# Kernel tuning notes

Hardware: AMD Instinct MI355X
Metric: run time of the kernel (lower is better)

Reference implementation:

```python
import jax, jax.numpy as jnp
import numpy as np

N, E, G = 20000, 320000, 256      # nodes, edges, graphs per batch
IN, D, P = 128, 256, 16           # input_dim, out_dim, n_prot
EPS, R, TEMP = 1e-7, 0.5, 0.2


def setup_inputs() -> dict:
    key = jax.random.key(0)
    ks = jax.random.split(key, 9)
    x = jax.random.normal(ks[0], (N, IN), jnp.float32)
    edge_index = jax.random.randint(ks[1], (2, E), 0, N)
    batch = jnp.sort(jax.random.randint(ks[2], (N,), 0, G))
    def w(k, sh):
        fan_in = sh[0]
        return jax.random.normal(k, sh, jnp.float32) * (1.0 / fan_in) ** 0.5
    return {
        "x": x, "edge_index": edge_index, "batch": batch,
        "W1": w(ks[3], (IN, D)), "b1": jnp.zeros((D,), jnp.float32),
        "W2": w(ks[4], (D, D)), "b2": jnp.zeros((D,), jnp.float32),
        "Wm1": w(ks[5], (2 * D, D)), "bm1": jnp.zeros((D,), jnp.float32),
        "Wm2": w(ks[6], (D, 1)), "bm2": jnp.zeros((1,), jnp.float32),
        "prototypes": jax.random.normal(ks[7], (P, D), jnp.float32),
    }


def _cosine(a, b):
    # prototype_distances: cosine similarity with zero-norm -> eps fixup (eval path, no softmax)
    na = jnp.linalg.norm(a, axis=1)
    na = jnp.where(na == 0, na + EPS, na)
    nb = jnp.linalg.norm(b, axis=1)
    nb = jnp.where(nb == 0, nb + EPS, nb)
    return jnp.einsum('ik,jk->ij', a, b) / (na[:, None] * nb[None, :])


def _encoder(x, src, dst, batch, W1, b1, W2, b2, atten=None):
    # 2-layer GIN: h' = relu((h + sum_{j->i} atten_ji * h_j) W + b); graph emb = sum pool
    def conv(h, W, b):
        msg = h[src]                                   # [E, d]
        if atten is not None:
            msg = msg * atten                          # [E, 1] broadcast
        agg = h + jax.ops.segment_sum(msg, dst, num_segments=N)
        return jax.nn.relu(agg @ W + b)
    h = conv(x, W1, b1)
    h = conv(h, W2, b2)
    g = jax.ops.segment_sum(h, batch, num_segments=G)  # [G, D]
    return g, h


def reference(x, edge_index, batch, W1, b1, W2, b2, Wm1, bm1, Wm2, bm2, prototypes):
    src, dst = edge_index[0], edge_index[1]
    graph_embs, node_embs = _encoder(x, src, dst, batch, W1, b1, W2, b2)

    # eval path: assign each graph to nearest prototype by cosine similarity
    sim0 = _cosine(graph_embs, prototypes)             # [G, P]
    assign_prot = jnp.argmax(sim0, axis=1)             # [G]

    # sample_subgraph (eval: plain sigmoid, no gumbel noise)
    node_proto = prototypes[assign_prot[batch]]        # [N, D]
    h = jnp.concatenate([node_embs, node_proto], axis=-1)
    node_prob = jax.nn.relu(h @ Wm1 + bm1) @ Wm2 + bm2  # [N, 1]
    node_bern = jax.nn.sigmoid(node_prob)              # [N, 1]
    edge_bern = node_bern[src] * node_bern[dst]        # [E, 1]

    x2 = x * node_bern
    subgraph_embs, _ = _encoder(x2, src, dst, batch, W1, b1, W2, b2, atten=edge_bern)

    similarity = _cosine(subgraph_embs, prototypes)    # [G, P]

    # NCE loss
    a2 = jnp.argmax(similarity, axis=1)
    onehot = jax.nn.one_hot(a2, P, dtype=similarity.dtype)
    se = jnp.exp(similarity / TEMP)
    pos = (se * onehot).sum(axis=1)
    neg = (se * (1.0 - onehot)).sum(axis=1)
    NCE_loss = -jnp.log(pos / neg).mean()

    # KL regularizers
    nb = node_bern
    KL_node = (nb * jnp.log(nb / R + EPS)
               + (1 - nb) * jnp.log((1 - nb) / (1 - R + EPS) + EPS)).mean()
    eb = edge_bern
    KL_edge = (eb * jnp.log(eb / (R * R) + EPS)
               + (1 - eb) * jnp.log((1 - eb) / (1 - R * R + EPS) + EPS)).mean()
    KL_loss = KL_node + KL_edge

    data_sim = _cosine(subgraph_embs, subgraph_embs)   # [G, G]
    return (KL_loss, NCE_loss, similarity, node_bern, edge_bern,
            data_sim, subgraph_embs, node_embs)
```

## Files before the change

kernel.cpp:

```cpp
#include <hip/hip_runtime.h>
#include <cmath>
#include <cstdint>

#define DINL __device__ __forceinline__

namespace {

constexpr int Nn = 20000, Ee = 320000, Gg = 256, Dd = 256, Pp = 16;
constexpr int Npad = 20096;
constexpr float EPSf = 1e-7f, Rf = 0.5f, TEMPf = 0.2f;

typedef unsigned short u16;
typedef __attribute__((ext_vector_type(8))) short short8;
typedef __attribute__((ext_vector_type(4))) float floatx4;
typedef __attribute__((ext_vector_type(2))) unsigned int u2v;
typedef __attribute__((ext_vector_type(4))) unsigned int u4v;

DINL float waveSum(float x) {
#pragma unroll
  for (int off = 32; off > 0; off >>= 1) x += __shfl_xor(x, off, 64);
  return x;
}

DINL u16 f2bf(float f) {
  unsigned u = __float_as_uint(f);
  unsigned r = u + 0x7fffu + ((u >> 16) & 1u);
  return (u16)(r >> 16);
}
DINL float bf2f(u16 h) { return __uint_as_float(((unsigned)h) << 16); }

__global__ void k_setup(const int* __restrict__ dst, int* __restrict__ deg,
                        const float* __restrict__ W1, const float* __restrict__ W2,
                        const float* __restrict__ Wm1, u16* __restrict__ W1th,
                        u16* __restrict__ W1tl, u16* __restrict__ W2th,
                        u16* __restrict__ W2tl, u16* __restrict__ Wm1th,
                        u16* __restrict__ Wm1tl, const float* __restrict__ proto,
                        const float* __restrict__ bm1, float* __restrict__ pcb,
                        float* __restrict__ pnorm, const float* __restrict__ x,
                        u16* __restrict__ xbf, const int* __restrict__ batch,
                        int* __restrict__ goff) {
  const int eB = (Ee + 255) / 256;
  int blk = blockIdx.x;
  int tid = threadIdx.x;
  if (blk < eB) {
    int e = blk * 256 + tid;
    if (e < Ee) atomicAdd(&deg[dst[e]], 1);
  } else if (blk < eB + 640) {
    int idx = (blk - eB) * 256 + tid;
    const float* W;
    u16 *th, *tl;
    int K;
    if (idx < 128 * 256) {
      W = W1; th = W1th; tl = W1tl; K = 128;
    } else if (idx < 128 * 256 + 256 * 256) {
      idx -= 128 * 256;
      W = W2; th = W2th; tl = W2tl; K = 256;
    } else {
      idx -= 128 * 256 + 256 * 256;
      W = Wm1; th = Wm1th; tl = Wm1tl; K = 256;
    }
    int k = idx >> 8, n = idx & 255;
    float v = W[idx];
    u16 h = f2bf(v);
    th[(size_t)n * K + k] = h;
    tl[(size_t)n * K + k] = f2bf(v - bf2f(h));
  } else if (blk < eB + 656) {
    int p = blk - eB - 640;
    float s = bm1[tid];
    for (int k = 0; k < Dd; k++)
      s += proto[p * Dd + k] * Wm1[(size_t)(Dd + k) * Dd + tid];
    pcb[p * Dd + tid] = s;
    if (tid < 64) {
      float4 v = ((const float4*)(proto + (size_t)p * Dd))[tid];
      float nsq = waveSum(v.x * v.x + v.y * v.y + v.z * v.z + v.w * v.w);
      if (tid == 0) {
        float n = sqrtf(nsq);
        pnorm[p] = (n == 0.f) ? EPSf : n;
      }
    }
  } else if (blk < eB + 656 + 2500) {
    int i = (blk - eB - 656) * 256 + tid;
    if (i < Nn * 128 / 4) {
      float4 v = ((const float4*)x)[i];
      u2v o;
      o.x = (unsigned)f2bf(v.x) | ((unsigned)f2bf(v.y) << 16);
      o.y = (unsigned)f2bf(v.z) | ((unsigned)f2bf(v.w) << 16);
      __builtin_nontemporal_store(o, (u2v*)&xbf[(size_t)i * 4]);
    }
  } else {
    for (int i = tid; i < Nn; i += 256) {
      int bi = batch[i];
      int bp = (i == 0) ? -1 : batch[i - 1];
      for (int g = bp + 1; g <= bi; ++g) goff[g] = i;
      if (i == Nn - 1)
        for (int g = bi + 1; g <= Gg; ++g) goff[g] = Nn;
    }
  }
}

__global__ __launch_bounds__(1024) void k_scan(const int* __restrict__ deg,
                                               int* __restrict__ offs) {
  __shared__ int part[1024];
  int tid = threadIdx.x;
  const int chunk = (Nn + 1023) >> 10;
  int start = tid * chunk;
  int s = 0;
  for (int k = 0; k < chunk; k++) { int i = start + k; if (i < Nn) s += deg[i]; }
  part[tid] = s;
  __syncthreads();
  for (int off = 1; off < 1024; off <<= 1) {
    int v = (tid >= off) ? part[tid - off] : 0;
    __syncthreads();
    part[tid] += v;
    __syncthreads();
  }
  int run = (tid == 0) ? 0 : part[tid - 1];
  for (int k = 0; k < chunk; k++) {
    int i = start + k;
    if (i < Nn) { offs[i] = run; run += deg[i]; }
  }
  if (start < Nn && start + chunk >= Nn) offs[Nn] = run;
}

__global__ void k_fill(const int* __restrict__ src, const int* __restrict__ dst,
                       const int* __restrict__ offs, int* __restrict__ cursor,
                       int* __restrict__ csr) {
  int e = blockIdx.x * 256 + threadIdx.x;
  if (e < Ee) {
    int d = dst[e];
    int pos = atomicAdd(&cursor[d], 1);
    csr[offs[d] + pos] = src[e];
  }
}

template <int DIM, int EPL, bool INBF>
DINL void slice(float r[EPL], const void* __restrict__ hv, int row, int ce) {
  if constexpr (INBF) {
    const u16* p = (const u16*)hv + (size_t)row * DIM + ce;
    ushort4 u = *(const ushort4*)p;
    r[0] = bf2f(u.x); r[1] = bf2f(u.y); r[2] = bf2f(u.z); r[3] = bf2f(u.w);
  } else {
    const float* p = (const float*)hv + (size_t)row * DIM + ce;
    float2 u = *(const float2*)p;
    r[0] = u.x; r[1] = u.y;
  }
}

template <int DIM, int MODE, bool INBF, bool OSPL>
__global__ __launch_bounds__(256) void k_aggc(
    const void* __restrict__ hv, const float* __restrict__ nb,
    const int* __restrict__ offs, const int* __restrict__ csr,
    u16* __restrict__ oh, u16* __restrict__ ol) {
  constexpr int EPL = INBF ? 4 : 2;
  constexpr int COLS = EPL * 16;
  constexpr int CHUNKS = DIM / COLS;
  int c = (int)(blockIdx.x % CHUNKS);
  int grp = (int)(blockIdx.x / CHUNKS);
  int wv = threadIdx.x >> 6, lane = threadIdx.x & 63;
  int sub = lane >> 4, l = lane & 15;
  int node = grp * 16 + wv * 4 + sub;
  if (node >= Nn) return;
  int ce = c * COLS + l * EPL;
  float self[EPL], ts[EPL];
  slice<DIM, EPL, INBF>(self, hv, node, ce);
#pragma unroll
  for (int j = 0; j < EPL; j++) ts[j] = 0.f;
  int beg = offs[node], end = offs[node + 1];
  int k = beg;
  for (; k + 4 <= end; k += 4) {
    int s0 = csr[k], s1 = csr[k + 1], s2 = csr[k + 2], s3 = csr[k + 3];
    float r0[EPL], r1[EPL], r2[EPL], r3[EPL];
    slice<DIM, EPL, INBF>(r0, hv, s0, ce);
    slice<DIM, EPL, INBF>(r1, hv, s1, ce);
    slice<DIM, EPL, INBF>(r2, hv, s2, ce);
    slice<DIM, EPL, INBF>(r3, hv, s3, ce);
    if (MODE == 0) {
#pragma unroll
      for (int j = 0; j < EPL; j++) ts[j] += (r0[j] + r1[j]) + (r2[j] + r3[j]);
    } else {
      float w0 = nb[s0], w1 = nb[s1], w2 = nb[s2], w3 = nb[s3];
      if (MODE == 1) { w0 *= w0; w1 *= w1; w2 *= w2; w3 *= w3; }
#pragma unroll
      for (int j = 0; j < EPL; j++)
        ts[j] += (w0 * r0[j] + w1 * r1[j]) + (w2 * r2[j] + w3 * r3[j]);
    }
  }
  for (; k < end; k++) {
    int s = csr[k];
    float r[EPL];
    slice<DIM, EPL, INBF>(r, hv, s, ce);
    if (MODE == 0) {
#pragma unroll
      for (int j = 0; j < EPL; j++) ts[j] += r[j];
    } else {
      float wq = nb[s];
      if (MODE == 1) wq *= wq;
#pragma unroll
      for (int j = 0; j < EPL; j++) ts[j] += wq * r[j];
    }
  }
  float val[EPL];
  if (MODE == 0) {
#pragma unroll
    for (int j = 0; j < EPL; j++) val[j] = self[j] + ts[j];
  } else if (MODE == 1) {
    float wi = nb[node];
#pragma unroll
    for (int j = 0; j < EPL; j++) val[j] = wi * (self[j] + ts[j]);
  } else {
    float wi = nb[node];
#pragma unroll
    for (int j = 0; j < EPL; j++) val[j] = self[j] + wi * ts[j];
  }
  u16 hs[EPL], ls[EPL];
#pragma unroll
  for (int j = 0; j < EPL; j++) {
    hs[j] = f2bf(val[j]);
    if (OSPL) ls[j] = f2bf(val[j] - bf2f(hs[j]));
  }
  u16* po = oh + (size_t)node * DIM + ce;
  if constexpr (EPL == 2) {
    unsigned v = (unsigned)hs[0] | ((unsigned)hs[1] << 16);
    __builtin_nontemporal_store(v, (unsigned*)po);
  } else {
    u2v v;
    v.x = (unsigned)hs[0] | ((unsigned)hs[1] << 16);
    v.y = (unsigned)hs[2] | ((unsigned)hs[3] << 16);
    __builtin_nontemporal_store(v, (u2v*)po);
  }
  if constexpr (OSPL) {
    u16* pl = ol + (size_t)node * DIM + ce;
    if constexpr (EPL == 2) {
      unsigned v = (unsigned)ls[0] | ((unsigned)ls[1] << 16);
      __builtin_nontemporal_store(v, (unsigned*)pl);
    } else {
      u2v v;
      v.x = (unsigned)ls[0] | ((unsigned)ls[1] << 16);
      v.y = (unsigned)ls[2] | ((unsigned)ls[3] << 16);
      __builtin_nontemporal_store(v, (u2v*)pl);
    }
  }
}

template <int K, bool SPLIT, bool AF32, int EPI>
__global__ __launch_bounds__(256) void k_mm(
    const void* __restrict__ Av, const u16* __restrict__ Al,
    const u16* __restrict__ Bh, const u16* __restrict__ Bl,
    const float* __restrict__ bias,
    float* __restrict__ outF, u16* __restrict__ outH,
    const float* __restrict__ pc, const int* __restrict__ batch,
    const int* __restrict__ assign, const float* __restrict__ Wm2,
    float* __restrict__ prob) {
  int b = (int)blockIdx.x;
  int g = b >> 5, lane5 = b & 31;
  int panel = g * 8 + (lane5 & 7);
  int col = lane5 >> 3;
  if (panel >= 157) return;
  int rowBase = panel * 128, colBase = col * 64;

  constexpr int SK = 40;
  __shared__ u16 AsH[128 * SK];
  __shared__ u16 AsL[SPLIT ? 128 * SK : 16];
  __shared__ u16 BsH[64 * SK];
  __shared__ u16 BsL[SPLIT ? 64 * SK : 16];
  __shared__ int ap_s[128];
  int t = threadIdx.x;
  if (EPI == 2 && t < 128) {
    int r = rowBase + t;
    ap_s[t] = (r < Nn) ? assign[batch[r]] : 0;
  }
  int lane = t & 63, wv = t >> 6;
  int quad = lane >> 4, l16 = lane & 15;
  int wm = wv * 32;
  floatx4 acc[2][4];
#pragma unroll
  for (int mt = 0; mt < 2; mt++)
#pragma unroll
    for (int nt = 0; nt < 4; nt++) acc[mt][nt] = (floatx4){0.f, 0.f, 0.f, 0.f};

  int ar = t >> 1;
  int ak = (t & 1) * 16;
  int bn = t >> 2;
  int bk = (t & 3) * 8;
  const u16* bgH = Bh + (size_t)(colBase + bn) * K + bk;
  const u16* bgL = Bl + (size_t)(colBase + bn) * K + bk;

  const u16* agH;
  const u16* agL;
  const float* agF;
  if constexpr (AF32) {
    agF = (const float*)Av + (size_t)(rowBase + ar) * K + ak;
  } else {
    agH = (const u16*)Av + (size_t)(rowBase + ar) * K + ak;
    agL = Al + (size_t)(rowBase + ar) * K + ak;
  }
  bool aok = AF32 ? (rowBase + ar < Nn) : true;

  u4v cA0, cA1, cA0l, cA1l, cB0, cB0l;
  float4 fA[4];
  if constexpr (AF32) {
#pragma unroll
    for (int q = 0; q < 4; q++)
      fA[q] = aok ? ((const float4*)agF)[q] : make_float4(0.f, 0.f, 0.f, 0.f);
  } else {
    cA0 = *(const u4v*)(agH);
    cA1 = *(const u4v*)(agH + 8);
    if constexpr (SPLIT) {
      cA0l = *(const u4v*)(agL);
      cA1l = *(const u4v*)(agL + 8);
    }
  }
  cB0 = *(const u4v*)(bgH);
  if constexpr (SPLIT) cB0l = *(const u4v*)(bgL);

  for (int k0 = 0; k0 < K; k0 += 32) {
    __syncthreads();
    if constexpr (AF32) {
      u16 hh[16], ll[16];
#pragma unroll
      for (int q = 0; q < 4; q++) {
        const float vv[4] = {fA[q].x, fA[q].y, fA[q].z, fA[q].w};
#pragma unroll
        for (int j = 0; j < 4; j++) {
          u16 h = f2bf(vv[j]);
          hh[q * 4 + j] = h;
          ll[q * 4 + j] = f2bf(vv[j] - bf2f(h));
        }
      }
      *(u4v*)&AsH[ar * SK + ak] = *(const u4v*)&hh[0];
      *(u4v*)&AsH[ar * SK + ak + 8] = *(const u4v*)&hh[8];
      *(u4v*)&AsL[ar * SK + ak] = *(const u4v*)&ll[0];
      *(u4v*)&AsL[ar * SK + ak + 8] = *(const u4v*)&ll[8];
    } else {
      *(u4v*)&AsH[ar * SK + ak] = cA0;
      *(u4v*)&AsH[ar * SK + ak + 8] = cA1;
      if constexpr (SPLIT) {
        *(u4v*)&AsL[ar * SK + ak] = cA0l;
        *(u4v*)&AsL[ar * SK + ak + 8] = cA1l;
      }
    }
    *(u4v*)&BsH[bn * SK + bk] = cB0;
    if constexpr (SPLIT) *(u4v*)&BsL[bn * SK + bk] = cB0l;
    __syncthreads();
    if (k0 + 32 < K) {
      if constexpr (AF32) {
#pragma unroll
        for (int q = 0; q < 4; q++)
          fA[q] = aok ? ((const float4*)(agF + k0 + 32))[q]
                      : make_float4(0.f, 0.f, 0.f, 0.f);
      } else {
        cA0 = *(const u4v*)(agH + k0 + 32);
        cA1 = *(const u4v*)(agH + k0 + 40);
        if constexpr (SPLIT) {
          cA0l = *(const u4v*)(agL + k0 + 32);
          cA1l = *(const u4v*)(agL + k0 + 40);
        }
      }
      cB0 = *(const u4v*)(bgH + k0 + 32);
      if constexpr (SPLIT) cB0l = *(const u4v*)(bgL + k0 + 32);
    }
    short8 aH[2], aL[2], bH[4], bL[4];
#pragma unroll
    for (int mt = 0; mt < 2; mt++) {
      int aoff = (wm + mt * 16 + l16) * SK + quad * 8;
      aH[mt] = *(const short8*)&AsH[aoff];
      if (SPLIT) aL[mt] = *(const short8*)&AsL[aoff];
    }
#pragma unroll
    for (int nt = 0; nt < 4; nt++) {
      int boff = (nt * 16 + l16) * SK + quad * 8;
      bH[nt] = *(const short8*)&BsH[boff];
      if (SPLIT) bL[nt] = *(const short8*)&BsL[boff];
    }
#pragma unroll
    for (int mt = 0; mt < 2; mt++)
#pragma unroll
      for (int nt = 0; nt < 4; nt++) {
        acc[mt][nt] = __builtin_amdgcn_mfma_f32_16x16x32_bf16(aH[mt], bH[nt], acc[mt][nt], 0, 0, 0);
        if constexpr (SPLIT) {
          acc[mt][nt] = __builtin_amdgcn_mfma_f32_16x16x32_bf16(aH[mt], bL[nt], acc[mt][nt], 0, 0, 0);
          acc[mt][nt] = __builtin_amdgcn_mfma_f32_16x16x32_bf16(aL[mt], bH[nt], acc[mt][nt], 0, 0, 0);
        }
      }
  }

  if constexpr (EPI == 0 || EPI == 1) {
#pragma unroll
    for (int mt = 0; mt < 2; mt++)
#pragma unroll
      for (int nt = 0; nt < 4; nt++) {
        int cc = colBase + nt * 16 + l16;
        float bv = bias[cc];
#pragma unroll
        for (int r = 0; r < 4; r++) {
          int row = rowBase + wm + mt * 16 + quad * 4 + r;
          if (row < Nn) {
            float v = fmaxf(acc[mt][nt][r] + bv, 0.f);
            if constexpr (EPI == 0) {
              outF[(size_t)row * 256 + cc] = v;
            } else {
              outH[(size_t)row * 256 + cc] = f2bf(v);
            }
          }
        }
      }
  } else {
#pragma unroll
    for (int mt = 0; mt < 2; mt++) {
      float part[4] = {0.f, 0.f, 0.f, 0.f};
#pragma unroll
      for (int nt = 0; nt < 4; nt++) {
        int cc = colBase + nt * 16 + l16;
        float wmv = Wm2[cc];
#pragma unroll
        for (int r = 0; r < 4; r++) {
          int ap = ap_s[wm + mt * 16 + quad * 4 + r];
          float tv = fmaxf(acc[mt][nt][r] + pc[ap * 256 + cc], 0.f);
          part[r] += tv * wmv;
        }
      }
#pragma unroll
      for (int r = 0; r < 4; r++) {
#pragma unroll
        for (int off = 1; off < 16; off <<= 1) part[r] += __shfl_xor(part[r], off, 64);
        if (l16 == 0) {
          int row = rowBase + wm + mt * 16 + quad * 4 + r;
          if (row < Nn) atomicAdd(&prob[row], part[r]);
        }
      }
    }
  }
}

__global__ __launch_bounds__(256) void k_poolassign(
    const float* __restrict__ h, const int* __restrict__ goff,
    const float* __restrict__ proto, const float* __restrict__ pnorm,
    int* __restrict__ assign) {
  __shared__ float row[Dd];
  int g = blockIdx.x, c = threadIdx.x;
  int beg = goff[g], end = goff[g + 1];
  float s = 0.f;
  for (int n = beg; n < end; ++n)
    s += __builtin_nontemporal_load(&h[(size_t)n * Dd + c]);
  row[c] = s;
  __syncthreads();
  if (c < 64) {
    float4 v = ((const float4*)row)[c];
    float na = sqrtf(waveSum(v.x * v.x + v.y * v.y + v.z * v.z + v.w * v.w));
    if (na == 0.f) na = EPSf;
    float best = -1e30f;
    int bi = 0;
#pragma unroll
    for (int p = 0; p < Pp; p++) {
      float4 w = *(const float4*)(proto + (size_t)p * Dd + c * 4);
      float d = waveSum(v.x * w.x + v.y * w.y + v.z * w.z + v.w * w.w);
      float sim = d / (na * pnorm[p]);
      if (sim > best) { best = sim; bi = p; }
    }
    if (c == 0) assign[g] = bi;
  }
}

__global__ __launch_bounds__(256) void k_poolsim(
    const float* __restrict__ h, const int* __restrict__ goff,
    const float* __restrict__ proto, const float* __restrict__ pnorm,
    float* __restrict__ o_sg, float* __restrict__ sgemb,
    float* __restrict__ osim, float* __restrict__ snorm,
    float* __restrict__ nceAcc) {
  __shared__ float row[Dd];
  int g = blockIdx.x, c = threadIdx.x;
  int beg = goff[g], end = goff[g + 1];
  float s = 0.f;
  for (int n = beg; n < end; ++n)
    s += __builtin_nontemporal_load(&h[(size_t)n * Dd + c]);
  row[c] = s;
  o_sg[(size_t)g * Dd + c] = s;
  sgemb[(size_t)g * Dd + c] = s;
  __syncthreads();
  if (c < 64) {
    float4 v = ((const float4*)row)[c];
    float na = sqrtf(waveSum(v.x * v.x + v.y * v.y + v.z * v.z + v.w * v.w));
    if (na == 0.f) na = EPSf;
    float sims[Pp];
#pragma unroll
    for (int p = 0; p < Pp; p++) {
      float4 w = *(const float4*)(proto + (size_t)p * Dd + c * 4);
      float d = waveSum(v.x * w.x + v.y * w.y + v.z * w.z + v.w * w.w);
      float sim = d / (na * pnorm[p]);
      sims[p] = sim;
      if (c == p) osim[g * Pp + p] = sim;
    }
    float best = sims[0];
    int bi = 0;
#pragma unroll
    for (int p = 1; p < Pp; p++) {
      if (sims[p] > best) { best = sims[p]; bi = p; }
    }
    float pos = 0.f, neg = 0.f;
#pragma unroll
    for (int p = 0; p < Pp; p++) {
      float e = expf(sims[p] / TEMPf);
      if (p == bi) pos = e; else neg += e;
    }
    if (c == 0) {
      atomicAdd(nceAcc, -logf(pos / neg));
      snorm[g] = na;
    }
  }
}

__global__ void k_berneb(const float* __restrict__ prob, const float* __restrict__ bm2,
                         const int* __restrict__ src, const int* __restrict__ dst,
                         float* __restrict__ ob, float* __restrict__ oe,
                         float* __restrict__ accs) {
  const int nB = (Nn + 255) / 256;
  int b = blockIdx.x;
  if (b < nB) {
    int i = b * 256 + threadIdx.x;
    float val = 0.f;
    if (i < Nn) {
      float z = prob[i] + bm2[0];
      float p = 1.f / (1.f + expf(-z));
      ob[i] = p;
      const float invA = 1.f / Rf, invB = 1.f / (1.f - Rf + EPSf);
      val = p * logf(p * invA + EPSf) + (1.f - p) * logf((1.f - p) * invB + EPSf);
    }
    val = waveSum(val);
    __shared__ float wsum[4];
    int lane = threadIdx.x & 63, wvv = threadIdx.x >> 6;
    if (lane == 0) wsum[wvv] = val;
    __syncthreads();
    if (threadIdx.x == 0) atomicAdd(accs, wsum[0] + wsum[1] + wsum[2] + wsum[3]);
  } else {
    int e = (b - nB) * 256 + threadIdx.x;
    float val = 0.f;
    if (e < Ee) {
      float zs = prob[src[e]] + bm2[0];
      float zd = prob[dst[e]] + bm2[0];
      float ps = 1.f / (1.f + expf(-zs));
      float pd = 1.f / (1.f + expf(-zd));
      float v = ps * pd;
      __builtin_nontemporal_store(v, &oe[e]);
      const float invA = 1.f / (Rf * Rf), invB = 1.f / (1.f - Rf * Rf + EPSf);
      val = v * logf(v * invA + EPSf) + (1.f - v) * logf((1.f - v) * invB + EPSf);
    }
    val = waveSum(val);
    __shared__ float wsum2[4];
    int lane = threadIdx.x & 63, wvv = threadIdx.x >> 6;
    if (lane == 0) wsum2[wvv] = val;
    __syncthreads();
    if (threadIdx.x == 0) atomicAdd(accs + 1, wsum2[0] + wsum2[1] + wsum2[2] + wsum2[3]);
  }
}

__global__ void k_datasim(const float* __restrict__ S, const float* __restrict__ snorm,
                          float* __restrict__ out, const float* __restrict__ accs,
                          float* __restrict__ o_kl, float* __restrict__ o_nce) {
  int i = blockIdx.x, j = threadIdx.x;
  if (i == 0 && j == 0) {
    o_kl[0] = accs[0] / (float)Nn + accs[1] / (float)Ee;
    o_nce[0] = accs[2] / (float)Gg;
  }
  __shared__ float si[Dd];
  si[j] = S[(size_t)i * Dd + j];
  __syncthreads();
  const float4* rj = (const float4*)(S + (size_t)j * Dd);
  const float4* sif = (const float4*)si;
  float d = 0.f;
#pragma unroll 4
  for (int k = 0; k < Dd / 4; k++) {
    float4 a = sif[k];
    float4 b = rj[k];
    d += a.x * b.x + a.y * b.y + a.z * b.z + a.w * b.w;
  }
  out[(size_t)i * Gg + j] = d / (snorm[i] * snorm[j]);
}

}

extern "C" void kernel_launch(void* const* d_in, const int* in_sizes, int n_in,
                              void* d_out, int out_size, void* d_ws, size_t ws_size,
                              hipStream_t stream) {
  const float* x = (const float*)d_in[0];
  const int* ei = (const int*)d_in[1];
  const int* batch = (const int*)d_in[2];
  const float* W1 = (const float*)d_in[3];
  const float* b1 = (const float*)d_in[4];
  const float* W2 = (const float*)d_in[5];
  const float* b2 = (const float*)d_in[6];
  const float* Wm1 = (const float*)d_in[7];
  const float* bm1 = (const float*)d_in[8];
  const float* Wm2 = (const float*)d_in[9];
  const float* bm2 = (const float*)d_in[10];
  const float* proto = (const float*)d_in[11];
  const int* src = ei;
  const int* dst = ei + Ee;

  float* out = (float*)d_out;
  float* o_kl = out;
  float* o_nce = out + 1;
  float* o_sim = out + 2;
  float* o_nb = o_sim + Gg * Pp;
  float* o_eb = o_nb + Nn;
  float* o_ds = o_eb + Ee;
  float* o_sg = o_ds + Gg * Gg;
  float* o_ne = o_sg + Gg * Dd;

  char* w = (char*)d_ws;
  auto take = [&](size_t bytes) -> char* {
    char* p = w;
    w += (bytes + 255) & ~(size_t)255;
    return p;
  };
  const size_t halfR = (size_t)Npad * 256 * 2;
  float* bufB = (float*)take((size_t)Npad * 256 * 4);
  char* R2 = take(2 * halfR);
  u16* A1h = (u16*)R2;
  u16* A1l = (u16*)(R2 + (size_t)Npad * 128 * 2);
  u16* A2h = (u16*)R2;
  u16* A2l = (u16*)(R2 + halfR);
  u16* h1b = (u16*)R2;
  u16* a2bh = (u16*)(R2 + halfR);
  u16* a1bh = (u16*)take((size_t)Npad * 128 * 2);
  u16* xbf = (u16*)take((size_t)Nn * 128 * 2);

  int* csr = (int*)take((size_t)Ee * 4);
  int* deg = (int*)take((size_t)Nn * 4);
  int* cursor = (int*)take((size_t)Nn * 4);
  float* prob = (float*)take(Nn * 4);
  float* accs = (float*)take(16);
  float* sgemb = (float*)take((size_t)Gg * Dd * 4);
  int* offs = (int*)take((size_t)(Nn + 1) * 4);
  int* goff = (int*)take((size_t)(Gg + 1) * 4);
  float* pcb = (float*)take((size_t)Pp * Dd * 4);
  float* pnorm = (float*)take(Pp * 4);
  int* assign = (int*)take(Gg * 4);
  float* snorm = (float*)take(Gg * 4);
  u16* W1th = (u16*)take((size_t)256 * 128 * 2);
  u16* W1tl = (u16*)take((size_t)256 * 128 * 2);
  u16* W2th = (u16*)take((size_t)256 * 256 * 2);
  u16* W2tl = (u16*)take((size_t)256 * 256 * 2);
  u16* Wm1th = (u16*)take((size_t)256 * 256 * 2);
  u16* Wm1tl = (u16*)take((size_t)256 * 256 * 2);

  hipMemsetAsync(deg, 0, 3 * 80128 + 256, stream);

  const int eB = (Ee + 255) / 256;
  const int nB = (Nn + 255) / 256;
  const int gmm = 640;

  k_setup<<<eB + 656 + 2500 + 1, 256, 0, stream>>>(
      dst, deg, W1, W2, Wm1, W1th, W1tl, W2th, W2tl, Wm1th, Wm1tl, proto, bm1,
      pcb, pnorm, x, xbf, batch, goff);
  k_scan<<<1, 1024, 0, stream>>>(deg, offs);
  k_fill<<<eB, 256, 0, stream>>>(src, dst, offs, cursor, csr);

  k_aggc<128, 0, false, true><<<1250 * 4, 256, 0, stream>>>(x, nullptr, offs, csr, A1h, A1l);
  k_mm<128, true, false, 0><<<gmm, 256, 0, stream>>>(A1h, A1l, W1th, W1tl, b1, bufB,
                                                     nullptr, nullptr, nullptr, nullptr,
                                                     nullptr, nullptr);
  k_aggc<256, 0, false, true><<<1250 * 8, 256, 0, stream>>>(bufB, nullptr, offs, csr, A2h, A2l);
  k_mm<256, true, false, 0><<<gmm, 256, 0, stream>>>(A2h, A2l, W2th, W2tl, b2, o_ne,
                                                     nullptr, nullptr, nullptr, nullptr,
                                                     nullptr, nullptr);
  k_poolassign<<<Gg, 256, 0, stream>>>(o_ne, goff, proto, pnorm, assign);
  k_mm<256, true, true, 2><<<gmm, 256, 0, stream>>>(o_ne, nullptr, Wm1th, Wm1tl,
                                                    nullptr, nullptr, nullptr, pcb,
                                                    batch, assign, Wm2, prob);
  k_berneb<<<nB + eB, 256, 0, stream>>>(prob, bm2, src, dst, o_nb, o_eb, accs);

  k_aggc<128, 1, true, false><<<1250 * 2, 256, 0, stream>>>(xbf, o_nb, offs, csr, a1bh, nullptr);
  k_mm<128, false, false, 1><<<gmm, 256, 0, stream>>>(a1bh, nullptr, W1th, nullptr, b1,
                                                      nullptr, h1b, nullptr, nullptr,
                                                      nullptr, nullptr, nullptr);
  k_aggc<256, 2, true, false><<<1250 * 4, 256, 0, stream>>>(h1b, o_nb, offs, csr, a2bh, nullptr);
  k_mm<256, false, false, 0><<<gmm, 256, 0, stream>>>(a2bh, nullptr, W2th, nullptr, b2,
                                                      bufB, nullptr, nullptr, nullptr,
                                                      nullptr, nullptr, nullptr);
  k_poolsim<<<Gg, 256, 0, stream>>>(bufB, goff, proto, pnorm, o_sg, sgemb, o_sim, snorm,
                                    accs + 2);
  k_datasim<<<Gg, 256, 0, stream>>>(sgemb, snorm, o_ds, accs, o_kl, o_nce);
}
```

Measured before the change: 451.3 us.

## Split setup kernel and redistribute preprocessing across the launch schedule

Breaks the monolithic setup kernel into a degree-count kernel, a merged scan/graph-offset kernel, and a separate weight-prep kernel. The x-to-bf16 conversion moves into the Bernoulli kernel, where its output is first needed. The aim is to shorten the critical path before CSR construction and to spread independent work into kernels with spare capacity. This adds one extra kernel launch and makes the Bernoulli kernel larger.

```diff
diff --git a/kernel.cpp b/kernel.cpp
--- a/kernel.cpp
+++ b/kernel.cpp
@@ -29,66 +29,38 @@
 }
 DINL float bf2f(u16 h) { return __uint_as_float(((unsigned)h) << 16); }
 
-__global__ void k_setup(const int* __restrict__ dst, int* __restrict__ deg,
-                        const float* __restrict__ W1, const float* __restrict__ W2,
-                        const float* __restrict__ Wm1, u16* __restrict__ W1th,
-                        u16* __restrict__ W1tl, u16* __restrict__ W2th,
-                        u16* __restrict__ W2tl, u16* __restrict__ Wm1th,
-                        u16* __restrict__ Wm1tl, const float* __restrict__ proto,
-                        const float* __restrict__ bm1, float* __restrict__ pcb,
-                        float* __restrict__ pnorm, const float* __restrict__ x,
-                        u16* __restrict__ xbf, const int* __restrict__ batch,
-                        int* __restrict__ goff) {
-  const int eB = (Ee + 255) / 256;
-  int blk = blockIdx.x;
+__global__ void k_deg(const int* __restrict__ dst, int* __restrict__ deg) {
+  int e = blockIdx.x * 256 + threadIdx.x;
+  if (e < Ee) atomicAdd(&deg[dst[e]], 1);
+}
+
+__global__ __launch_bounds__(1024) void k_pre(const int* __restrict__ deg,
+                                              int* __restrict__ offs,
+                                              const int* __restrict__ batch,
+                                              int* __restrict__ goff) {
   int tid = threadIdx.x;
-  if (blk < eB) {
-    int e = blk * 256 + tid;
-    if (e < Ee) atomicAdd(&deg[dst[e]], 1);
-  } else if (blk < eB + 640) {
-    int idx = (blk - eB) * 256 + tid;
-    const float* W;
-    u16 *th, *tl;
-    int K;
-    if (idx < 128 * 256) {
-      W = W1; th = W1th; tl = W1tl; K = 128;
-    } else if (idx < 128 * 256 + 256 * 256) {
-      idx -= 128 * 256;
-      W = W2; th = W2th; tl = W2tl; K = 256;
-    } else {
-      idx -= 128 * 256 + 256 * 256;
-      W = Wm1; th = Wm1th; tl = Wm1tl; K = 256;
-    }
-    int k = idx >> 8, n = idx & 255;
-    float v = W[idx];
-    u16 h = f2bf(v);
-    th[(size_t)n * K + k] = h;
-    tl[(size_t)n * K + k] = f2bf(v - bf2f(h));
-  } else if (blk < eB + 656) {
-    int p = blk - eB - 640;
-    float s = bm1[tid];
-    for (int k = 0; k < Dd; k++)
-      s += proto[p * Dd + k] * Wm1[(size_t)(Dd + k) * Dd + tid];
-    pcb[p * Dd + tid] = s;
-    if (tid < 64) {
-      float4 v = ((const float4*)(proto + (size_t)p * Dd))[tid];
-      float nsq = waveSum(v.x * v.x + v.y * v.y + v.z * v.z + v.w * v.w);
-      if (tid == 0) {
-        float n = sqrtf(nsq);
-        pnorm[p] = (n == 0.f) ? EPSf : n;
-      }
-    }
-  } else if (blk < eB + 656 + 2500) {
-    int i = (blk - eB - 656) * 256 + tid;
-    if (i < Nn * 128 / 4) {
-      float4 v = ((const float4*)x)[i];
-      u2v o;
-      o.x = (unsigned)f2bf(v.x) | ((unsigned)f2bf(v.y) << 16);
-      o.y = (unsigned)f2bf(v.z) | ((unsigned)f2bf(v.w) << 16);
-      __builtin_nontemporal_store(o, (u2v*)&xbf[(size_t)i * 4]);
-    }
-  } else {
-    for (int i = tid; i < Nn; i += 256) {
+  if (blockIdx.x == 0) {
+    __shared__ int part[1024];
+    const int chunk = (Nn + 1023) >> 10;
+    int start = tid * chunk;
+    int s = 0;
+    for (int k = 0; k < chunk; k++) { int i = start + k; if (i < Nn) s += deg[i]; }
+    part[tid] = s;
+    __syncthreads();
+    for (int off = 1; off < 1024; off <<= 1) {
+      int v = (tid >= off) ? part[tid - off] : 0;
+      __syncthreads();
+      part[tid] += v;
+      __syncthreads();
+    }
+    int run = (tid == 0) ? 0 : part[tid - 1];
+    for (int k = 0; k < chunk; k++) {
+      int i = start + k;
+      if (i < Nn) { offs[i] = run; run += deg[i]; }
+    }
+    if (start < Nn && start + chunk >= Nn) offs[Nn] = run;
+  } else {
+    for (int i = tid; i < Nn; i += 1024) {
       int bi = batch[i];
       int bp = (i == 0) ? -1 : batch[i - 1];
       for (int g = bp + 1; g <= bi; ++g) goff[g] = i;
@@ -96,30 +68,6 @@
         for (int g = bi + 1; g <= Gg; ++g) goff[g] = Nn;
     }
   }
-}
-
-__global__ __launch_bounds__(1024) void k_scan(const int* __restrict__ deg,
-                                               int* __restrict__ offs) {
-  __shared__ int part[1024];
-  int tid = threadIdx.x;
-  const int chunk = (Nn + 1023) >> 10;
-  int start = tid * chunk;
-  int s = 0;
-  for (int k = 0; k < chunk; k++) { int i = start + k; if (i < Nn) s += deg[i]; }
-  part[tid] = s;
-  __syncthreads();
-  for (int off = 1; off < 1024; off <<= 1) {
-    int v = (tid >= off) ? part[tid - off] : 0;
-    __syncthreads();
-    part[tid] += v;
-    __syncthreads();
-  }
-  int run = (tid == 0) ? 0 : part[tid - 1];
-  for (int k = 0; k < chunk; k++) {
-    int i = start + k;
-    if (i < Nn) { offs[i] = run; run += deg[i]; }
-  }
-  if (start < Nn && start + chunk >= Nn) offs[Nn] = run;
 }
 
 __global__ void k_fill(const int* __restrict__ src, const int* __restrict__ dst,
@@ -131,6 +79,51 @@
     int pos = atomicAdd(&cursor[d], 1);
     csr[offs[d] + pos] = src[e];
   }
+}
+
+__global__ void k_prep(const float* __restrict__ W1, const float* __restrict__ W2,
+                       const float* __restrict__ Wm1, u16* __restrict__ W1th,
+                       u16* __restrict__ W1tl, u16* __restrict__ W2th,
+                       u16* __restrict__ W2tl, u16* __restrict__ Wm1th,
+                       u16* __restrict__ Wm1tl, const float* __restrict__ proto,
+                       const float* __restrict__ bm1, float* __restrict__ pcb,
+                       float* __restrict__ pnorm) {
+  int blk = blockIdx.x;
+  if (blk >= 640) {
+    int p = blk - 640, t = threadIdx.x;
+    float s = bm1[t];
+    for (int k = 0; k < Dd; k++)
+      s += proto[p * Dd + k] * Wm1[(size_t)(Dd + k) * Dd + t];
+    pcb[p * Dd + t] = s;
+    if (t < 64) {
+      float4 v = ((const float4*)(proto + (size_t)p * Dd))[t];
+      float nsq = waveSum(v.x * v.x + v.y * v.y + v.z * v.z + v.w * v.w);
+      if (t == 0) {
+        float n = sqrtf(nsq);
+        pnorm[p] = (n == 0.f) ? EPSf : n;
+      }
+    }
+    return;
+  }
+  int idx = blk * 256 + threadIdx.x;
+  const float* W;
+  u16 *th, *tl;
+  int K;
+  if (idx < 128 * 256) {
+    W = W1; th = W1th; tl = W1tl; K = 128;
+  } else if (idx < 128 * 256 + 256 * 256) {
+    idx -= 128 * 256;
+    W = W2; th = W2th; tl = W2tl; K = 256;
+  } else {
+    idx -= 128 * 256 + 256 * 256;
+    if (idx >= 256 * 256) return;
+    W = Wm1; th = Wm1th; tl = Wm1tl; K = 256;
+  }
+  int k = idx >> 8, n = idx & 255;
+  float v = W[idx];
+  u16 h = f2bf(v);
+  th[(size_t)n * K + k] = h;
+  tl[(size_t)n * K + k] = f2bf(v - bf2f(h));
 }
 
 template <int DIM, int EPL, bool INBF>
@@ -511,9 +504,10 @@
 
 __global__ void k_berneb(const float* __restrict__ prob, const float* __restrict__ bm2,
                          const int* __restrict__ src, const int* __restrict__ dst,
+                         const float* __restrict__ x, u16* __restrict__ xbf,
                          float* __restrict__ ob, float* __restrict__ oe,
                          float* __restrict__ accs) {
-  const int nB = (Nn + 255) / 256;
+  const int nB = (Nn + 255) / 256, eB = (Ee + 255) / 256;
   int b = blockIdx.x;
   if (b < nB) {
     int i = b * 256 + threadIdx.x;
@@ -531,7 +525,7 @@
     if (lane == 0) wsum[wvv] = val;
     __syncthreads();
     if (threadIdx.x == 0) atomicAdd(accs, wsum[0] + wsum[1] + wsum[2] + wsum[3]);
-  } else {
+  } else if (b < nB + eB) {
     int e = (b - nB) * 256 + threadIdx.x;
     float val = 0.f;
     if (e < Ee) {
@@ -550,6 +544,15 @@
     if (lane == 0) wsum2[wvv] = val;
     __syncthreads();
     if (threadIdx.x == 0) atomicAdd(accs + 1, wsum2[0] + wsum2[1] + wsum2[2] + wsum2[3]);
+  } else {
+    int i = (b - nB - eB) * 256 + threadIdx.x;
+    if (i < Nn * 128 / 4) {
+      float4 v = ((const float4*)x)[i];
+      u2v o;
+      o.x = (unsigned)f2bf(v.x) | ((unsigned)f2bf(v.y) << 16);
+      o.y = (unsigned)f2bf(v.z) | ((unsigned)f2bf(v.w) << 16);
+      __builtin_nontemporal_store(o, (u2v*)&xbf[(size_t)i * 4]);
+    }
   }
 }
 
@@ -649,11 +652,11 @@
   const int nB = (Nn + 255) / 256;
   const int gmm = 640;
 
-  k_setup<<<eB + 656 + 2500 + 1, 256, 0, stream>>>(
-      dst, deg, W1, W2, Wm1, W1th, W1tl, W2th, W2tl, Wm1th, Wm1tl, proto, bm1,
-      pcb, pnorm, x, xbf, batch, goff);
-  k_scan<<<1, 1024, 0, stream>>>(deg, offs);
+  k_deg<<<eB, 256, 0, stream>>>(dst, deg);
+  k_pre<<<2, 1024, 0, stream>>>(deg, offs, batch, goff);
   k_fill<<<eB, 256, 0, stream>>>(src, dst, offs, cursor, csr);
+  k_prep<<<656, 256, 0, stream>>>(W1, W2, Wm1, W1th, W1tl, W2th, W2tl, Wm1th, Wm1tl,
+                                  proto, bm1, pcb, pnorm);
 
   k_aggc<128, 0, false, true><<<1250 * 4, 256, 0, stream>>>(x, nullptr, offs, csr, A1h, A1l);
   k_mm<128, true, false, 0><<<gmm, 256, 0, stream>>>(A1h, A1l, W1th, W1tl, b1, bufB,
@@ -667,7 +670,8 @@
   k_mm<256, true, true, 2><<<gmm, 256, 0, stream>>>(o_ne, nullptr, Wm1th, Wm1tl,
                                                     nullptr, nullptr, nullptr, pcb,
                                                     batch, assign, Wm2, prob);
-  k_berneb<<<nB + eB, 256, 0, stream>>>(prob, bm2, src, dst, o_nb, o_eb, accs);
+  k_berneb<<<nB + eB + (Nn * 128 / 4 + 255) / 256, 256, 0, stream>>>(
+      prob, bm2, src, dst, x, xbf, o_nb, o_eb, accs);
 
   k_aggc<128, 1, true, false><<<1250 * 2, 256, 0, stream>>>(xbf, o_nb, offs, csr, a1bh, nullptr);
   k_mm<128, false, false, 1><<<gmm, 256, 0, stream>>>(a1bh, nullptr, W1th, nullptr, b1,
```

Result: faster. 435.3 us (-3.5%).
